# Kernel optimization log

Measured on AMD Instinct MI355X. Metric: run time of the kernel, lower is better.

## Reference

```python
import jax, jax.numpy as jnp
import numpy as np

N_EXPERTS = 8
TOP_K = 2
W_SCALE = 0.02


def setup_inputs() -> dict:
    key = jax.random.key(0)
    ks = jax.random.split(key, 4)
    S, B, D, F = 2048, 2, 1024, 4096
    x = jax.random.normal(ks[0], (S, B, D), dtype=jnp.float32)
    gate_w = jax.random.normal(ks[1], (D, N_EXPERTS), dtype=jnp.float32) * W_SCALE
    gate_b = jnp.zeros((N_EXPERTS,), dtype=jnp.float32)
    w1 = jax.random.normal(ks[2], (N_EXPERTS, D, F), dtype=jnp.float32) * W_SCALE
    b1 = jnp.zeros((N_EXPERTS, F), dtype=jnp.float32)
    w2 = jax.random.normal(ks[3], (N_EXPERTS, F, D), dtype=jnp.float32) * W_SCALE
    b2 = jnp.zeros((N_EXPERTS, D), dtype=jnp.float32)
    return {"x": x, "gate_w": gate_w, "gate_b": gate_b,
            "w1": w1, "b1": b1, "w2": w2, "b2": b2}


def reference(x, gate_w, gate_b, w1, b1, w2, b2):
    # gate logits: [S, B, E]
    logits = jnp.einsum('sbd,de->sbe', x, gate_w) + gate_b
    top_w, top_idx = jax.lax.top_k(logits, TOP_K)            # [S,B,K]
    # softmax over the top-k logits in float32 (matches dtype=torch.float)
    probs = jax.nn.softmax(top_w.astype(jnp.float32), axis=-1)
    # dense combine weights [S, B, E]: zero for non-selected experts
    comb = jnp.sum(jax.nn.one_hot(top_idx, N_EXPERTS, dtype=probs.dtype)
                   * probs[..., None], axis=-2)
    out = jnp.zeros_like(x)
    for e in range(N_EXPERTS):  # fixed small structural loop over experts
        h = jax.nn.relu(jnp.einsum('sbd,df->sbf', x, w1[e]) + b1[e])
        y = jnp.einsum('sbf,fd->sbd', h, w2[e]) + b2[e]
        out = out + comb[..., e:e + 1].astype(x.dtype) * y
    return out
```

## Files before the change

### kernel.cpp

```cpp
#include <hip/hip_runtime.h>
#include <stdint.h>

#define T_TOK 4096
#define D_DIM 1024
#define F_DIM 4096
#define NEXP 8
#define BM 128
#define BN 128
#define BK 32
#define CAP 10240
#define MT256 (CAP / 256)
#define MT128 (CAP / 128)

typedef __attribute__((ext_vector_type(8))) short short8;
typedef __attribute__((ext_vector_type(4))) float f4;
typedef __attribute__((ext_vector_type(4))) unsigned short us4;

#define WS_SBASE   64
#define WS_TBASE   96
#define WS_TB128   160
#define WS_TOPI    256
#define WS_TOPP    (WS_TOPI + T_TOK*2*4)
#define WS_PSLOT   (WS_TOPP + T_TOK*2*4)
#define WS_XG      102400
#define WS_H       (WS_XG + (size_t)CAP*D_DIM*2)
#define WS_WT      (WS_H + (size_t)CAP*F_DIM*2)

__device__ __forceinline__ unsigned short f2bf(float f) {
    union { float f; uint32_t u; } c; c.f = f;
    uint32_t r = c.u + 0x7FFFu + ((c.u >> 16) & 1u);
    return (unsigned short)(r >> 16);
}
__device__ __forceinline__ float bf2f(unsigned short h) {
    union { uint32_t u; float f; } c; c.u = ((uint32_t)h) << 16;
    return c.f;
}

__global__ __launch_bounds__(256) void gate_kernel(
    const float* __restrict__ x, const float* __restrict__ gw,
    const float* __restrict__ gb,
    int* __restrict__ top_idx, float* __restrict__ top_p)
{
    int lane = threadIdx.x & 63;
    int t = blockIdx.x * 4 + (threadIdx.x >> 6);
    const float* xr = x + (size_t)t * D_DIM;
    float acc[8] = {0.f,0.f,0.f,0.f,0.f,0.f,0.f,0.f};
    for (int i = 0; i < 16; ++i) {
        int d = lane + i * 64;
        float xv = xr[d];
        const float* g = gw + d * 8;
        #pragma unroll
        for (int e = 0; e < 8; ++e) acc[e] += xv * g[e];
    }
    #pragma unroll
    for (int e = 0; e < 8; ++e) {
        #pragma unroll
        for (int off = 32; off > 0; off >>= 1)
            acc[e] += __shfl_xor(acc[e], off, 64);
    }
    if (lane == 0) {
        float l[8];
        #pragma unroll
        for (int e = 0; e < 8; ++e) l[e] = acc[e] + gb[e];
        int i0 = 0; float m0 = l[0];
        #pragma unroll
        for (int e = 1; e < 8; ++e) if (l[e] > m0) { m0 = l[e]; i0 = e; }
        int i1 = -1; float m1 = -3.4e38f;
        #pragma unroll
        for (int e = 0; e < 8; ++e) if (e != i0 && l[e] > m1) { m1 = l[e]; i1 = e; }
        float p0 = 1.f / (1.f + expf(m1 - m0));
        top_idx[t*2]   = i0; top_idx[t*2+1] = i1;
        top_p[t*2]     = p0; top_p[t*2+1]   = 1.f - p0;
    }
}

__global__ __launch_bounds__(256) void plan_kernel(
    const int* __restrict__ top_idx, int* __restrict__ sbase,
    int* __restrict__ tbase256, int* __restrict__ tbase128,
    int* __restrict__ pslot)
{
    __shared__ int woff[4][8];
    __shared__ int sb_s[8];
    int t = threadIdx.x, wv = t >> 6, lane = t & 63;
    int base = t * 32;

    int h[8] = {0,0,0,0,0,0,0,0};
    for (int i = 0; i < 32; ++i) {
        int e = top_idx[base + i];
        #pragma unroll
        for (int ee = 0; ee < 8; ++ee) h[ee] += (e == ee) ? 1 : 0;
    }
    int inc[8];
    #pragma unroll
    for (int ee = 0; ee < 8; ++ee) {
        int v = h[ee];
        #pragma unroll
        for (int off = 1; off < 64; off <<= 1) {
            int n = __shfl_up(v, off, 64);
            if (lane >= off) v += n;
        }
        inc[ee] = v;
    }
    if (lane == 63) {
        #pragma unroll
        for (int ee = 0; ee < 8; ++ee) woff[wv][ee] = inc[ee];
    }
    __syncthreads();
    if (t == 0) {
        int cnt[8];
        #pragma unroll
        for (int ee = 0; ee < 8; ++ee) {
            int s = 0;
            #pragma unroll
            for (int w = 0; w < 4; ++w) { int v = woff[w][ee]; woff[w][ee] = s; s += v; }
            cnt[ee] = s;
        }
        int b = 0, t2 = 0, t1 = 0;
        tbase256[0] = 0; tbase128[0] = 0;
        #pragma unroll
        for (int e = 0; e < 8; ++e) {
            sb_s[e] = b; sbase[e] = b;
            int m2 = (cnt[e] + 255) / 256;
            b  += m2 * 256;
            t2 += m2;
            t1 += m2 * 2;
            tbase256[e + 1] = t2;
            tbase128[e + 1] = t1;
        }
    }
    __syncthreads();
    int run[8];
    #pragma unroll
    for (int ee = 0; ee < 8; ++ee)
        run[ee] = sb_s[ee] + woff[wv][ee] + inc[ee] - h[ee];
    for (int i = 0; i < 32; ++i) {
        int e = top_idx[base + i];
        int slot = 0;
        #pragma unroll
        for (int ee = 0; ee < 8; ++ee) slot += (e == ee) ? run[ee] : 0;
        pslot[base + i] = slot;
        #pragma unroll
        for (int ee = 0; ee < 8; ++ee) run[ee] += (e == ee) ? 1 : 0;
    }
}

__global__ __launch_bounds__(256) void gather_kernel(
    const float* __restrict__ x, const int* __restrict__ pslot,
    uint16_t* __restrict__ xg)
{
    int t = blockIdx.x;
    int s0 = pslot[2*t], s1 = pslot[2*t + 1];
    int i = threadIdx.x;
    f4 v = ((const f4*)(x + (size_t)t * D_DIM))[i];
    us4 o;
    o.x = f2bf(v[0]); o.y = f2bf(v[1]); o.z = f2bf(v[2]); o.w = f2bf(v[3]);
    *(us4*)(xg + (size_t)s0 * D_DIM + i * 4) = o;
    *(us4*)(xg + (size_t)s1 * D_DIM + i * 4) = o;
}

__global__ __launch_bounds__(512) void convT_kernel(
    const float* __restrict__ W, uint16_t* __restrict__ WT, int K, int N)
{
    __shared__ float ts[64][65];
    int e = blockIdx.z;
    int n0 = blockIdx.x * 64, k0 = blockIdx.y * 64;
    const float* src = W + (size_t)e * K * N + (size_t)k0 * N + n0;
    int t = threadIdx.x;
    int kk = t >> 3, j = t & 7;
    f4 v0 = *(const f4*)(src + (size_t)kk * N + j * 8);
    f4 v1 = *(const f4*)(src + (size_t)kk * N + j * 8 + 4);
    #pragma unroll
    for (int i = 0; i < 4; ++i) ts[j*8 + i][kk] = v0[i];
    #pragma unroll
    for (int i = 0; i < 4; ++i) ts[j*8 + 4 + i][kk] = v1[i];
    __syncthreads();
    int nn = t >> 3;
    short8 o;
    #pragma unroll
    for (int i = 0; i < 8; ++i) o[i] = (short)f2bf(ts[nn][j*8 + i]);
    *(short8*)(WT + (size_t)e * N * K + (size_t)(n0 + nn) * K + k0 + j * 8) = o;
}

template<bool RELU>
__global__ __launch_bounds__(256, 3) void moe_gemm3(
    const uint16_t* __restrict__ A, const uint16_t* __restrict__ Bt,
    const float* __restrict__ bias, uint16_t* __restrict__ Cc,
    const int* __restrict__ tbase, const int* __restrict__ sbase,
    int K, int N, int NT)
{
    __shared__ uint16_t As3[3][BM][BK];
    __shared__ uint16_t Bs3[3][BN][BK];

    int nwg = gridDim.x;
    int lin = blockIdx.x;
    int wg = (lin & 7) * (nwg >> 3) + (lin >> 3);
    int q = wg >> 2;
    int nt = q % NT;
    int mt = (wg & 3) + (q / NT) * 4;

    if (mt >= tbase[8]) return;
    int e = 0;
    while (mt >= tbase[e + 1]) ++e;
    int row0 = sbase[e] + (mt - tbase[e]) * BM;
    int n0 = nt * BN;
    const uint16_t* Be = Bt + (size_t)e * N * K + (size_t)n0 * K;

    int tid = threadIdx.x;
    int wid = tid >> 6, lane = tid & 63;
    int wrow = (wid >> 1) * 64, wcol = (wid & 1) * 64;

    f4 acc[4][4] = {};

    int ovb = tid * 16;
    int rowA[2], koffA[2];
    #pragma unroll
    for (int j = 0; j < 2; ++j) {
        int ov = ovb + j * 4096;
        int row = ov >> 6;
        int cb  = (ov >> 4) & 3;
        rowA[j]  = row;
        koffA[j] = (cb ^ ((row >> 1) & 3)) << 3;
    }

    int abyte[4], bbyte[4];
    #pragma unroll
    for (int m = 0; m < 4; ++m) {
        int r = wrow + m * 16 + (lane & 15);
        abyte[m] = r * 64 + ((((lane >> 4) ^ ((r >> 1) & 3))) << 4);
    }
    #pragma unroll
    for (int n = 0; n < 4; ++n) {
        int c = wcol + n * 16 + (lane & 15);
        bbyte[n] = c * 64 + ((((lane >> 4) ^ ((c >> 1) & 3))) << 4);
    }
    const char* As0 = (const char*)&As3[0][0][0];
    const char* Bs0 = (const char*)&Bs3[0][0][0];

    auto STAGE = [&](int buf, int kt) {
        #pragma unroll
        for (int j = 0; j < 2; ++j) {
            const uint16_t* gpA = A + (size_t)(row0 + rowA[j]) * K + kt + koffA[j];
            __builtin_amdgcn_global_load_lds(
                (const __attribute__((address_space(1))) void*)gpA,
                (__attribute__((address_space(3))) void*)((char*)&As3[buf][0][0] + ovb + j * 4096),
                16, 0, 0);
            const uint16_t* gpB = Be + (size_t)rowA[j] * K + kt + koffA[j];
            __builtin_amdgcn_global_load_lds(
                (const __attribute__((address_space(1))) void*)gpB,
                (__attribute__((address_space(3))) void*)((char*)&Bs3[buf][0][0] + ovb + j * 4096),
                16, 0, 0);
        }
    };

    int nkt = K / BK;
    STAGE(0, 0);
    STAGE(1, BK);
    asm volatile("s_waitcnt vmcnt(4)" ::: "memory");
    __builtin_amdgcn_s_barrier();

    int buf = 0;
    for (int t = 0; t < nkt; ++t) {
        int cb = buf * 8192;
        short8 af[4], bfr[4];
        #pragma unroll
        for (int m = 0; m < 4; ++m) af[m] = *(const short8*)(As0 + cb + abyte[m]);
        #pragma unroll
        for (int n = 0; n < 4; ++n) bfr[n] = *(const short8*)(Bs0 + cb + bbyte[n]);

        bool stg = (t + 2) < nkt;
        if (stg) {
            int b2 = buf + 2; if (b2 >= 3) b2 -= 3;
            STAGE(b2, (t + 2) * BK);
        }

        #pragma unroll
        for (int m = 0; m < 4; ++m)
            #pragma unroll
            for (int n = 0; n < 4; ++n)
                acc[m][n] = __builtin_amdgcn_mfma_f32_16x16x32_bf16(
                    af[m], bfr[n], acc[m][n], 0, 0, 0);

        if (stg) asm volatile("s_waitcnt vmcnt(4)" ::: "memory");
        else     asm volatile("s_waitcnt vmcnt(0)" ::: "memory");
        __builtin_amdgcn_s_barrier();
        buf = (buf + 1 == 3) ? 0 : buf + 1;
    }

    #pragma unroll
    for (int n = 0; n < 4; ++n) {
        int c = wcol + n * 16 + (lane & 15);
        float bv = bias[(size_t)e * N + n0 + c];
        #pragma unroll
        for (int m = 0; m < 4; ++m) {
            int rb = wrow + m * 16 + (lane >> 4) * 4;
            #pragma unroll
            for (int r = 0; r < 4; ++r) {
                float v = acc[m][n][r] + bv;
                if (RELU) v = fmaxf(v, 0.f);
                Cc[(size_t)(row0 + rb + r) * N + n0 + c] = f2bf(v);
            }
        }
    }
}

template<bool RELU>
__global__ __launch_bounds__(256, 2) void moe_gemm5(
    const uint16_t* __restrict__ A, const uint16_t* __restrict__ Bt,
    const float* __restrict__ bias, uint16_t* __restrict__ Cc,
    const int* __restrict__ tbase, const int* __restrict__ sbase,
    int K, int N, int NT)
{
    __shared__ uint16_t As3[3][256][BK];
    __shared__ uint16_t Bs3[3][BN][BK];

    int nwg = gridDim.x;
    int lin = blockIdx.x;
    int wg = (lin & 7) * (nwg >> 3) + (lin >> 3);
    int q = wg >> 2;
    int nt = q % NT;
    int mt = (wg & 3) + (q / NT) * 4;

    if (mt >= tbase[8]) return;
    int e = 0;
    while (mt >= tbase[e + 1]) ++e;
    int row0 = sbase[e] + (mt - tbase[e]) * 256;
    int n0 = nt * BN;
    const uint16_t* Be = Bt + (size_t)e * N * K + (size_t)n0 * K;

    int tid = threadIdx.x;
    int wid = tid >> 6, lane = tid & 63;
    int wr = wid >> 1, wc = wid & 1;
    int lq = lane >> 4, lr = lane & 15;

    f4 acc[8][4] = {};

    int ovb = tid * 16;
    int rowS[4], koffS[4];
    #pragma unroll
    for (int j = 0; j < 4; ++j) {
        int ov = ovb + j * 4096;
        int row = ov >> 6;
        int cb  = (ov >> 4) & 3;
        rowS[j]  = row;
        koffS[j] = (cb ^ ((row >> 1) & 3)) << 3;
    }

    int abyte[8], bbyte[4];
    #pragma unroll
    for (int m = 0; m < 8; ++m) {
        int r = wr * 128 + m * 16 + lr;
        abyte[m] = r * 64 + (((lq ^ ((r >> 1) & 3))) << 4);
    }
    #pragma unroll
    for (int n = 0; n < 4; ++n) {
        int c = wc * 64 + n * 16 + lr;
        bbyte[n] = c * 64 + (((lq ^ ((c >> 1) & 3))) << 4);
    }
    const char* As0 = (const char*)&As3[0][0][0];
    const char* Bs0 = (const char*)&Bs3[0][0][0];

    auto STAGE = [&](int buf, int kt) {
        #pragma unroll
        for (int j = 0; j < 4; ++j) {
            const uint16_t* gpA = A + (size_t)(row0 + rowS[j]) * K + kt + koffS[j];
            __builtin_amdgcn_global_load_lds(
                (const __attribute__((address_space(1))) void*)gpA,
                (__attribute__((address_space(3))) void*)((char*)&As3[buf][0][0] + ovb + j * 4096),
                16, 0, 0);
        }
        #pragma unroll
        for (int j = 0; j < 2; ++j) {
            const uint16_t* gpB = Be + (size_t)rowS[j] * K + kt + koffS[j];
            __builtin_amdgcn_global_load_lds(
                (const __attribute__((address_space(1))) void*)gpB,
                (__attribute__((address_space(3))) void*)((char*)&Bs3[buf][0][0] + ovb + j * 4096),
                16, 0, 0);
        }
    };

    int nkt = K / BK;
    STAGE(0, 0);
    STAGE(1, BK);
    asm volatile("s_waitcnt vmcnt(6)" ::: "memory");
    __builtin_amdgcn_s_barrier();

    int buf = 0;
    for (int t = 0; t < nkt; ++t) {
        int cba = buf * 16384, cbb = buf * 8192;
        short8 af[8], bfr[4];
        #pragma unroll
        for (int m = 0; m < 8; ++m) af[m] = *(const short8*)(As0 + cba + abyte[m]);
        #pragma unroll
        for (int n = 0; n < 4; ++n) bfr[n] = *(const short8*)(Bs0 + cbb + bbyte[n]);

        bool stg = (t + 2) < nkt;
        if (stg) {
            int b2 = buf + 2; if (b2 >= 3) b2 -= 3;
            STAGE(b2, (t + 2) * BK);
        }

        #pragma unroll
        for (int m = 0; m < 8; ++m)
            #pragma unroll
            for (int n = 0; n < 4; ++n)
                acc[m][n] = __builtin_amdgcn_mfma_f32_16x16x32_bf16(
                    af[m], bfr[n], acc[m][n], 0, 0, 0);

        if (stg) asm volatile("s_waitcnt vmcnt(6)" ::: "memory");
        else     asm volatile("s_waitcnt vmcnt(0)" ::: "memory");
        __builtin_amdgcn_s_barrier();
        buf = (buf + 1 == 3) ? 0 : buf + 1;
    }

    #pragma unroll
    for (int n = 0; n < 4; ++n) {
        int c = wc * 64 + n * 16 + lr;
        float bv = bias[(size_t)e * N + n0 + c];
        #pragma unroll
        for (int m = 0; m < 8; ++m) {
            int rb = wr * 128 + m * 16 + lq * 4;
            #pragma unroll
            for (int r = 0; r < 4; ++r) {
                float v = acc[m][n][r] + bv;
                if (RELU) v = fmaxf(v, 0.f);
                Cc[(size_t)(row0 + rb + r) * N + n0 + c] = f2bf(v);
            }
        }
    }
}

__global__ __launch_bounds__(256) void combine_kernel(
    const uint16_t* __restrict__ Y, const int* __restrict__ pair_slot,
    const float* __restrict__ top_p, float* __restrict__ out)
{
    int t = blockIdx.x;
    int s0 = pair_slot[t*2], s1 = pair_slot[t*2+1];
    float p0 = top_p[t*2],  p1 = top_p[t*2+1];
    int i = threadIdx.x * 4;
    us4 a = *(const us4*)(Y + (size_t)s0 * D_DIM + i);
    us4 b = *(const us4*)(Y + (size_t)s1 * D_DIM + i);
    f4 o;
    o[0] = p0 * bf2f(a.x) + p1 * bf2f(b.x);
    o[1] = p0 * bf2f(a.y) + p1 * bf2f(b.y);
    o[2] = p0 * bf2f(a.z) + p1 * bf2f(b.z);
    o[3] = p0 * bf2f(a.w) + p1 * bf2f(b.w);
    *(f4*)(out + (size_t)t * D_DIM + i) = o;
}

extern "C" void kernel_launch(void* const* d_in, const int* in_sizes, int n_in,
                              void* d_out, int out_size, void* d_ws, size_t ws_size,
                              hipStream_t stream)
{
    const float* x  = (const float*)d_in[0];
    const float* gw = (const float*)d_in[1];
    const float* gb = (const float*)d_in[2];
    const float* w1 = (const float*)d_in[3];
    const float* b1 = (const float*)d_in[4];
    const float* w2 = (const float*)d_in[5];
    const float* b2 = (const float*)d_in[6];
    float* out = (float*)d_out;

    char* ws = (char*)d_ws;
    int*   sbase = (int*)(ws + WS_SBASE);
    int*   tb256 = (int*)(ws + WS_TBASE);
    int*   tb128 = (int*)(ws + WS_TB128);
    int*   topi  = (int*)(ws + WS_TOPI);
    float* topp  = (float*)(ws + WS_TOPP);
    int*   pslot = (int*)(ws + WS_PSLOT);
    uint16_t* xg = (uint16_t*)(ws + WS_XG);
    uint16_t* H  = (uint16_t*)(ws + WS_H);
    uint16_t* Y  = xg;
    uint16_t* WT = (uint16_t*)(ws + WS_WT);

    gate_kernel<<<T_TOK / 4, 256, 0, stream>>>(x, gw, gb, topi, topp);
    plan_kernel<<<1, 256, 0, stream>>>(topi, sbase, tb256, tb128, pslot);
    gather_kernel<<<T_TOK, 256, 0, stream>>>(x, pslot, xg);

    convT_kernel<<<dim3(F_DIM/64, D_DIM/64, NEXP), 512, 0, stream>>>(w1, WT, D_DIM, F_DIM);
    moe_gemm5<true ><<<MT256 * (F_DIM / BN), 256, 0, stream>>>(
        xg, WT, b1, H, tb256, sbase, D_DIM, F_DIM, F_DIM / BN);
    convT_kernel<<<dim3(D_DIM/64, F_DIM/64, NEXP), 512, 0, stream>>>(w2, WT, F_DIM, D_DIM);
    moe_gemm3<false><<<MT128 * (D_DIM / BN), 256, 0, stream>>>(
        H, WT, b2, Y, tb128, sbase, F_DIM, D_DIM, D_DIM / BN);

    combine_kernel<<<T_TOK, 256, 0, stream>>>(Y, pslot, topp, out);
}
```

Measured before the change: 307.8 us.

## Switch first expert GEMM to 128x256 tiles with 8 waves and 128-row padding

```diff
diff --git a/kernel.cpp b/kernel.cpp
--- a/kernel.cpp
+++ b/kernel.cpp
@@ -7,10 +7,10 @@
 #define NEXP 8
 #define BM 128
 #define BN 128
+#define BN2 256
 #define BK 32
-#define CAP 10240
-#define MT256 (CAP / 256)
-#define MT128 (CAP / 128)
+#define CAP 9216
+#define MT_MAX (CAP / BM)
 
 typedef __attribute__((ext_vector_type(8))) short short8;
 typedef __attribute__((ext_vector_type(4))) float f4;
@@ -18,13 +18,13 @@
 
 #define WS_SBASE   64
 #define WS_TBASE   96
-#define WS_TB128   160
 #define WS_TOPI    256
 #define WS_TOPP    (WS_TOPI + T_TOK*2*4)
 #define WS_PSLOT   (WS_TOPP + T_TOK*2*4)
 #define WS_XG      102400
 #define WS_H       (WS_XG + (size_t)CAP*D_DIM*2)
-#define WS_WT      (WS_H + (size_t)CAP*F_DIM*2)
+#define WS_Y       (WS_H + (size_t)CAP*F_DIM*2)
+#define WS_WT      (WS_Y + (size_t)CAP*D_DIM*2)
 
 __device__ __forceinline__ unsigned short f2bf(float f) {
     union { float f; uint32_t u; } c; c.f = f;
@@ -76,8 +76,7 @@
 
 __global__ __launch_bounds__(256) void plan_kernel(
     const int* __restrict__ top_idx, int* __restrict__ sbase,
-    int* __restrict__ tbase256, int* __restrict__ tbase128,
-    int* __restrict__ pslot)
+    int* __restrict__ tbase, int* __restrict__ pslot)
 {
     __shared__ int woff[4][8];
     __shared__ int sb_s[8];
@@ -115,17 +114,14 @@
             for (int w = 0; w < 4; ++w) { int v = woff[w][ee]; woff[w][ee] = s; s += v; }
             cnt[ee] = s;
         }
-        int b = 0, t2 = 0, t1 = 0;
-        tbase256[0] = 0; tbase128[0] = 0;
+        int b = 0, tb0 = 0;
+        tbase[0] = 0;
         #pragma unroll
         for (int e = 0; e < 8; ++e) {
             sb_s[e] = b; sbase[e] = b;
-            int m2 = (cnt[e] + 255) / 256;
-            b  += m2 * 256;
-            t2 += m2;
-            t1 += m2 * 2;
-            tbase256[e + 1] = t2;
-            tbase128[e + 1] = t1;
+            int mt = (cnt[e] + BM - 1) / BM;
+            b += mt * BM; tb0 += mt;
+            tbase[e + 1] = tb0;
         }
     }
     __syncthreads();
@@ -304,14 +300,14 @@
 }
 
 template<bool RELU>
-__global__ __launch_bounds__(256, 2) void moe_gemm5(
+__global__ __launch_bounds__(512, 4) void moe_gemm6(
     const uint16_t* __restrict__ A, const uint16_t* __restrict__ Bt,
     const float* __restrict__ bias, uint16_t* __restrict__ Cc,
     const int* __restrict__ tbase, const int* __restrict__ sbase,
     int K, int N, int NT)
 {
-    __shared__ uint16_t As3[3][256][BK];
-    __shared__ uint16_t Bs3[3][BN][BK];
+    __shared__ uint16_t As3[3][BM][BK];
+    __shared__ uint16_t Bs3[3][BN2][BK];
 
     int nwg = gridDim.x;
     int lin = blockIdx.x;
@@ -323,57 +319,54 @@
     if (mt >= tbase[8]) return;
     int e = 0;
     while (mt >= tbase[e + 1]) ++e;
-    int row0 = sbase[e] + (mt - tbase[e]) * 256;
-    int n0 = nt * BN;
+    int row0 = sbase[e] + (mt - tbase[e]) * BM;
+    int n0 = nt * BN2;
     const uint16_t* Be = Bt + (size_t)e * N * K + (size_t)n0 * K;
 
     int tid = threadIdx.x;
     int wid = tid >> 6, lane = tid & 63;
-    int wr = wid >> 1, wc = wid & 1;
+    int wrow = (wid >> 2) * 64, wcol = (wid & 3) * 64;
     int lq = lane >> 4, lr = lane & 15;
 
-    f4 acc[8][4] = {};
+    f4 acc[4][4] = {};
 
     int ovb = tid * 16;
-    int rowS[4], koffS[4];
-    #pragma unroll
-    for (int j = 0; j < 4; ++j) {
-        int ov = ovb + j * 4096;
+    int rowS[2], koffS[2];
+    #pragma unroll
+    for (int j = 0; j < 2; ++j) {
+        int ov = ovb + j * 8192;
         int row = ov >> 6;
         int cb  = (ov >> 4) & 3;
         rowS[j]  = row;
         koffS[j] = (cb ^ ((row >> 1) & 3)) << 3;
     }
 
-    int abyte[8], bbyte[4];
-    #pragma unroll
-    for (int m = 0; m < 8; ++m) {
-        int r = wr * 128 + m * 16 + lr;
+    int abyte[4], bbyte[4];
+    #pragma unroll
+    for (int m = 0; m < 4; ++m) {
+        int r = wrow + m * 16 + lr;
         abyte[m] = r * 64 + (((lq ^ ((r >> 1) & 3))) << 4);
     }
     #pragma unroll
     for (int n = 0; n < 4; ++n) {
-        int c = wc * 64 + n * 16 + lr;
+        int c = wcol + n * 16 + lr;
         bbyte[n] = c * 64 + (((lq ^ ((c >> 1) & 3))) << 4);
     }
     const char* As0 = (const char*)&As3[0][0][0];
     const char* Bs0 = (const char*)&Bs3[0][0][0];
 
     auto STAGE = [&](int buf, int kt) {
-        #pragma unroll
-        for (int j = 0; j < 4; ++j) {
-            const uint16_t* gpA = A + (size_t)(row0 + rowS[j]) * K + kt + koffS[j];
-            __builtin_amdgcn_global_load_lds(
-                (const __attribute__((address_space(1))) void*)gpA,
-                (__attribute__((address_space(3))) void*)((char*)&As3[buf][0][0] + ovb + j * 4096),
-                16, 0, 0);
-        }
+        const uint16_t* gpA = A + (size_t)(row0 + rowS[0]) * K + kt + koffS[0];
+        __builtin_amdgcn_global_load_lds(
+            (const __attribute__((address_space(1))) void*)gpA,
+            (__attribute__((address_space(3))) void*)((char*)&As3[buf][0][0] + ovb),
+            16, 0, 0);
         #pragma unroll
         for (int j = 0; j < 2; ++j) {
             const uint16_t* gpB = Be + (size_t)rowS[j] * K + kt + koffS[j];
             __builtin_amdgcn_global_load_lds(
                 (const __attribute__((address_space(1))) void*)gpB,
-                (__attribute__((address_space(3))) void*)((char*)&Bs3[buf][0][0] + ovb + j * 4096),
+                (__attribute__((address_space(3))) void*)((char*)&Bs3[buf][0][0] + ovb + j * 8192),
                 16, 0, 0);
         }
     };
@@ -381,15 +374,15 @@
     int nkt = K / BK;
     STAGE(0, 0);
     STAGE(1, BK);
-    asm volatile("s_waitcnt vmcnt(6)" ::: "memory");
+    asm volatile("s_waitcnt vmcnt(3)" ::: "memory");
     __builtin_amdgcn_s_barrier();
 
     int buf = 0;
     for (int t = 0; t < nkt; ++t) {
-        int cba = buf * 16384, cbb = buf * 8192;
-        short8 af[8], bfr[4];
-        #pragma unroll
-        for (int m = 0; m < 8; ++m) af[m] = *(const short8*)(As0 + cba + abyte[m]);
+        int cba = buf * 8192, cbb = buf * 16384;
+        short8 af[4], bfr[4];
+        #pragma unroll
+        for (int m = 0; m < 4; ++m) af[m] = *(const short8*)(As0 + cba + abyte[m]);
         #pragma unroll
         for (int n = 0; n < 4; ++n) bfr[n] = *(const short8*)(Bs0 + cbb + bbyte[n]);
 
@@ -400,13 +393,13 @@
         }
 
         #pragma unroll
-        for (int m = 0; m < 8; ++m)
+        for (int m = 0; m < 4; ++m)
             #pragma unroll
             for (int n = 0; n < 4; ++n)
                 acc[m][n] = __builtin_amdgcn_mfma_f32_16x16x32_bf16(
                     af[m], bfr[n], acc[m][n], 0, 0, 0);
 
-        if (stg) asm volatile("s_waitcnt vmcnt(6)" ::: "memory");
+        if (stg) asm volatile("s_waitcnt vmcnt(3)" ::: "memory");
         else     asm volatile("s_waitcnt vmcnt(0)" ::: "memory");
         __builtin_amdgcn_s_barrier();
         buf = (buf + 1 == 3) ? 0 : buf + 1;
@@ -414,11 +407,11 @@
 
     #pragma unroll
     for (int n = 0; n < 4; ++n) {
-        int c = wc * 64 + n * 16 + lr;
+        int c = wcol + n * 16 + lr;
         float bv = bias[(size_t)e * N + n0 + c];
         #pragma unroll
-        for (int m = 0; m < 8; ++m) {
-            int rb = wr * 128 + m * 16 + lq * 4;
+        for (int m = 0; m < 4; ++m) {
+            int rb = wrow + m * 16 + lq * 4;
             #pragma unroll
             for (int r = 0; r < 4; ++r) {
                 float v = acc[m][n][r] + bv;
@@ -462,26 +455,25 @@
 
     char* ws = (char*)d_ws;
     int*   sbase = (int*)(ws + WS_SBASE);
-    int*   tb256 = (int*)(ws + WS_TBASE);
-    int*   tb128 = (int*)(ws + WS_TB128);
+    int*   tbase = (int*)(ws + WS_TBASE);
     int*   topi  = (int*)(ws + WS_TOPI);
     float* topp  = (float*)(ws + WS_TOPP);
     int*   pslot = (int*)(ws + WS_PSLOT);
     uint16_t* xg = (uint16_t*)(ws + WS_XG);
     uint16_t* H  = (uint16_t*)(ws + WS_H);
-    uint16_t* Y  = xg;
+    uint16_t* Y  = (uint16_t*)(ws + WS_Y);
     uint16_t* WT = (uint16_t*)(ws + WS_WT);
 
     gate_kernel<<<T_TOK / 4, 256, 0, stream>>>(x, gw, gb, topi, topp);
-    plan_kernel<<<1, 256, 0, stream>>>(topi, sbase, tb256, tb128, pslot);
+    plan_kernel<<<1, 256, 0, stream>>>(topi, sbase, tbase, pslot);
     gather_kernel<<<T_TOK, 256, 0, stream>>>(x, pslot, xg);
 
     convT_kernel<<<dim3(F_DIM/64, D_DIM/64, NEXP), 512, 0, stream>>>(w1, WT, D_DIM, F_DIM);
-    moe_gemm5<true ><<<MT256 * (F_DIM / BN), 256, 0, stream>>>(
-        xg, WT, b1, H, tb256, sbase, D_DIM, F_DIM, F_DIM / BN);
+    moe_gemm6<true ><<<MT_MAX * (F_DIM / BN2), 512, 0, stream>>>(
+        xg, WT, b1, H, tbase, sbase, D_DIM, F_DIM, F_DIM / BN2);
     convT_kernel<<<dim3(D_DIM/64, F_DIM/64, NEXP), 512, 0, stream>>>(w2, WT, F_DIM, D_DIM);
-    moe_gemm3<false><<<MT128 * (D_DIM / BN), 256, 0, stream>>>(
-        H, WT, b2, Y, tb128, sbase, F_DIM, D_DIM, D_DIM / BN);
+    moe_gemm3<false><<<MT_MAX * (D_DIM / BN), 256, 0, stream>>>(
+        H, WT, b2, Y, tbase, sbase, F_DIM, D_DIM, D_DIM / BN);
 
     combine_kernel<<<T_TOK, 256, 0, stream>>>(Y, pslot, topp, out);
 }
```

New measurement: 296.4 us. -3.7%, faster.
